# Kernel tuning notes

Hardware: AMD Instinct MI355X
Metric: run time of the kernel (lower is better)

The kernel has to match this reference:

```python
import jax, jax.numpy as jnp
import numpy as np

DIM = 64
B, H, W = 4, 80, 80


def setup_inputs() -> dict:
    key = jax.random.key(0)
    k1, k2, k3 = jax.random.split(key, 3)
    x = jax.random.normal(k1, (B, DIM, H, W), dtype=jnp.float32)
    # 1x1 conv == per-pixel linear: weight [3*dim, dim], bias [3*dim]
    w_qkv = jax.random.normal(k2, (3 * DIM, DIM), dtype=jnp.float32) * (1.0 / np.sqrt(DIM).astype(np.float32))
    b_qkv = jax.random.normal(k3, (3 * DIM,), dtype=jnp.float32) * 0.01
    return {"x": x, "w_qkv": w_qkv, "b_qkv": b_qkv}


def reference(x, w_qkv, b_qkv):
    Bb, C, Hh, Ww = x.shape
    N = Hh * Ww
    # 1x1 conv -> qkv, chunked along channels
    qkv = jnp.einsum('bchw,oc->bohw', x, w_qkv) + b_qkv[None, :, None, None]
    q, k, v = jnp.split(qkv, 3, axis=1)  # each [B,C,H,W]

    # --- spatial attention (uses q on both sides, as in the original) ---
    # qk: transpose(3,1) -> [B,W,H,C] -> [B, W*H, C]
    qk = jnp.transpose(q, (0, 3, 2, 1)).reshape(Bb, N, C)
    # kq: [B, C, H*W]  (note: different flatten order than qk, faithful to source)
    kq = q.reshape(Bb, C, N)
    ms = jax.nn.softmax(jnp.matmul(qk, kq), axis=-1)  # [B, N, N]

    # --- channel attention ---
    kf = k.reshape(Bb, C, N)                                # [B, C, N]
    qf = jnp.transpose(q, (0, 3, 2, 1)).reshape(Bb, N, C)   # [B, N, C]
    ma = jax.nn.softmax(jnp.matmul(kf, qf), axis=-1)        # [B, C, C]

    # --- apply to v ---
    vq = jnp.transpose(v, (0, 3, 2, 1)).reshape(Bb, N, C)   # [B, N, C]
    ms_out = jnp.matmul(ms, vq)                             # [B, N, C]
    ms_out = jnp.swapaxes(ms_out, 1, 2).reshape(Bb, C, Hh, Ww)
    ma_out = jnp.matmul(ma, v.reshape(Bb, C, N)).reshape(Bb, C, Hh, Ww)
    return ms_out + ma_out
```

## Files before the change

### kernel.cpp

```cpp
#include <hip/hip_runtime.h>
#include <stdint.h>

#define BATCH 4
#define CH 64
#define HW 80
#define NPIX 6400
#define SPLITS 3

typedef __attribute__((ext_vector_type(8))) short bf16x8;
typedef __attribute__((ext_vector_type(4))) float f32x4;

#define QSCALE 1.2011224087864498f
#define ESHIFT 115.41560327111707f

static __device__ __forceinline__ unsigned short f2bf(float f) {
  union { float f; unsigned int u; } v; v.f = f;
  unsigned int u = v.u;
  return (unsigned short)((u + 0x7fffu + ((u >> 16) & 1u)) >> 16);
}
static __device__ __forceinline__ float bf2f(unsigned short h) {
  union { unsigned int u; float f; } v; v.u = ((unsigned int)h) << 16;
  return v.f;
}
static __device__ __forceinline__ unsigned int split_pack(float a) {
  unsigned short hi = f2bf(a);
  union { unsigned int u; float f; } hf; hf.u = ((unsigned int)hi) << 16;
  unsigned short lo = f2bf(a - hf.f);
  return (unsigned int)hi | ((unsigned int)lo << 16);
}
static __device__ __forceinline__ void deint(uint4 a, uint4 b, bf16x8* h, bf16x8* l) {
  union { unsigned int u[4]; bf16x8 v; } H, L;
  H.u[0] = __builtin_amdgcn_perm(a.y, a.x, 0x05040100u);
  H.u[1] = __builtin_amdgcn_perm(a.w, a.z, 0x05040100u);
  H.u[2] = __builtin_amdgcn_perm(b.y, b.x, 0x05040100u);
  H.u[3] = __builtin_amdgcn_perm(b.w, b.z, 0x05040100u);
  L.u[0] = __builtin_amdgcn_perm(a.y, a.x, 0x07060302u);
  L.u[1] = __builtin_amdgcn_perm(a.w, a.z, 0x07060302u);
  L.u[2] = __builtin_amdgcn_perm(b.y, b.x, 0x07060302u);
  L.u[3] = __builtin_amdgcn_perm(b.w, b.z, 0x07060302u);
  *h = H.v; *l = L.v;
}

__global__ __launch_bounds__(512) void qkv_kernel(
    const float* __restrict__ x, const float* __restrict__ w,
    const float* __restrict__ bias, unsigned short* __restrict__ Qtbf,
    unsigned short* __restrict__ Vbf, unsigned int* __restrict__ Kpk,
    unsigned int* __restrict__ Qtn) {
  __shared__ float qs[64][65];
  int bid = blockIdx.x;
  int b = bid / 100, tile = bid % 100;
  int p0 = tile * 64;
  int t = threadIdx.x;
  int i = t & 63;
  int og = __builtin_amdgcn_readfirstlane(t >> 6);
  int p = p0 + i;
  int tp = (p % HW) * HW + p / HW;
  const float* xb = x + (size_t)b * CH * NPIX + p;
  float xv[64];
#pragma unroll
  for (int c = 0; c < 64; ++c) xv[c] = xb[(size_t)c * NPIX];
  size_t bc = (size_t)b * CH * NPIX;
  for (int j = 0; j < 24; j += 4) {
    int o = og * 24 + j;
    const float* wr0 = w + o * 64;
    const float* wr1 = wr0 + 64;
    const float* wr2 = wr0 + 128;
    const float* wr3 = wr0 + 192;
    float a0 = bias[o], a1 = bias[o + 1], a2 = bias[o + 2], a3 = bias[o + 3];
#pragma unroll
    for (int c = 0; c < 64; ++c) {
      float xc = xv[c];
      a0 += wr0[c] * xc;
      a1 += wr1[c] * xc;
      a2 += wr2[c] * xc;
      a3 += wr3[c] * xc;
    }
    float av[4] = {a0, a1, a2, a3};
#pragma unroll
    for (int u = 0; u < 4; ++u) {
      int oo = o + u;
      int cc = oo & 63;
      int kind = oo >> 6;
      float a = av[u];
      if (kind == 0) {
        qs[cc][i] = a;
        Qtn[bc + (size_t)cc * NPIX + tp] = split_pack(a);
      } else if (kind == 1) {
        Kpk[bc + (size_t)cc * NPIX + p] = split_pack(a);
      } else {
        Vbf[bc + (size_t)cc * NPIX + p] = f2bf(a);
      }
    }
  }
  __syncthreads();
  int j2 = t >> 3, g = t & 7;
  int pj = p0 + j2;
  int tpj = (pj % HW) * HW + pj / HW;
  unsigned int pk4[4];
#pragma unroll
  for (int q4 = 0; q4 < 4; ++q4) {
    float a0 = qs[g * 8 + q4 * 2][j2] * QSCALE;
    float a1 = qs[g * 8 + q4 * 2 + 1][j2] * QSCALE;
    pk4[q4] = (unsigned int)f2bf(a0) | ((unsigned int)f2bf(a1) << 16);
  }
  unsigned short* dst = Qtbf + ((size_t)b * NPIX + tpj) * 64 + g * 8;
  uint4 w0 = {pk4[0], pk4[1], pk4[2], pk4[3]};
  *(uint4*)&dst[0] = w0;
}

__global__ __launch_bounds__(256) void gram_kernel(
    const unsigned int* __restrict__ Kpk, const unsigned int* __restrict__ Qtn,
    float* __restrict__ Pc) {
  int bid = blockIdx.x;
  int b = bid / 100, chunk = bid % 100;
  int n0 = chunk * 64;
  int t = threadIdx.x;
  int w = t >> 6, lane = t & 63;
  int quad = lane >> 4, l16 = lane & 15;
  size_t bc = (size_t)b * CH * NPIX;

  f32x4 acc[4];
#pragma unroll
  for (int ct = 0; ct < 4; ++ct) acc[ct] = (f32x4){0.f, 0.f, 0.f, 0.f};

  const unsigned int* kp = Kpk + bc + (size_t)(w * 16 + l16) * NPIX + n0;
  bf16x8 ah[2], al[2];
#pragma unroll
  for (int ks2 = 0; ks2 < 2; ++ks2) {
    uint4 ua = *(const uint4*)&kp[ks2 * 32 + quad * 8];
    uint4 ub = *(const uint4*)&kp[ks2 * 32 + quad * 8 + 4];
    deint(ua, ub, &ah[ks2], &al[ks2]);
  }
#pragma unroll
  for (int ct = 0; ct < 4; ++ct) {
    const unsigned int* qp = Qtn + bc + (size_t)(ct * 16 + l16) * NPIX + n0;
#pragma unroll
    for (int ks2 = 0; ks2 < 2; ++ks2) {
      uint4 va = *(const uint4*)&qp[ks2 * 32 + quad * 8];
      uint4 vb = *(const uint4*)&qp[ks2 * 32 + quad * 8 + 4];
      bf16x8 bh, bl;
      deint(va, vb, &bh, &bl);
      acc[ct] = __builtin_amdgcn_mfma_f32_16x16x32_bf16(ah[ks2], bh, acc[ct], 0, 0, 0);
      acc[ct] = __builtin_amdgcn_mfma_f32_16x16x32_bf16(ah[ks2], bl, acc[ct], 0, 0, 0);
      acc[ct] = __builtin_amdgcn_mfma_f32_16x16x32_bf16(al[ks2], bh, acc[ct], 0, 0, 0);
    }
  }
#pragma unroll
  for (int ct = 0; ct < 4; ++ct)
#pragma unroll
    for (int r = 0; r < 4; ++r)
      atomicAdd(&Pc[((size_t)b * 64 + w * 16 + quad * 4 + r) * 64 + ct * 16 + l16],
                acc[ct][r]);
}

__global__ __launch_bounds__(256) void flash_kernel(
    const unsigned short* __restrict__ Qtbf, const unsigned short* __restrict__ Vbf,
    float* __restrict__ Opart, float* __restrict__ Lpart) {
  __shared__ char smem[40960] __attribute__((aligned(128)));

  int bid = blockIdx.x;
  int b = bid / 300;
  int rem = bid % 300;
  int qt = rem / 3, split = rem % 3;
  int p0 = qt * 64;
  int t = threadIdx.x;
  int w = t >> 6, lane = t & 63;
  int quad = lane >> 4, l16 = lane & 15;
  int sw = l16 & 7;
  size_t bq = (size_t)b * NPIX;
  size_t bC = (size_t)b * CH * NPIX;

  bf16x8 aq[2];
#pragma unroll
  for (int ks = 0; ks < 2; ++ks)
    aq[ks] = *(const bf16x8*)&Qtbf[(bq + p0 + w * 16 + l16) * 64 + ks * 32 + quad * 8];

  f32x4 oacc[4];
#pragma unroll
  for (int ct = 0; ct < 4; ++ct) oacc[ct] = (f32x4){0.f, 0.f, 0.f, 0.f};
  float psum = 0.f;

  const unsigned short* Kb = Qtbf + bq * 64;
  const unsigned short* Vb = Vbf + bC;
  int r0 = t >> 3, s0 = t & 7;
  int r1 = r0 + 32;
  int wOff0 = r0 * 64 + ((s0 ^ (r0 & 7)) << 3);
  int wOff1 = r1 * 64 + ((s0 ^ (r1 & 7)) << 3);

  int kt0 = split * 34;
  int niter = (split == 2) ? 32 : 34;

  unsigned short* Pw = (unsigned short*)(smem + 32768) + w * 16 * 64;

  uint4 kreg0, kreg1, vreg0, vreg1;
  {
    int n0 = kt0 * 64;
    kreg0 = *(const uint4*)&Kb[(size_t)(n0 + r0) * 64 + s0 * 8];
    vreg0 = *(const uint4*)&Vb[(size_t)r0 * NPIX + n0 + s0 * 8];
    kreg1 = *(const uint4*)&Kb[(size_t)(n0 + r1) * 64 + s0 * 8];
    vreg1 = *(const uint4*)&Vb[(size_t)r1 * NPIX + n0 + s0 * 8];
  }
  {
    unsigned short* K0 = (unsigned short*)smem;
    unsigned short* V0 = (unsigned short*)(smem + 16384);
    *(uint4*)&K0[wOff0] = kreg0;
    *(uint4*)&V0[wOff0] = vreg0;
    *(uint4*)&K0[wOff1] = kreg1;
    *(uint4*)&V0[wOff1] = vreg1;
  }
  {
    int n1 = (kt0 + 1) * 64;
    kreg0 = *(const uint4*)&Kb[(size_t)(n1 + r0) * 64 + s0 * 8];
    vreg0 = *(const uint4*)&Vb[(size_t)r0 * NPIX + n1 + s0 * 8];
    kreg1 = *(const uint4*)&Kb[(size_t)(n1 + r1) * 64 + s0 * 8];
    vreg1 = *(const uint4*)&Vb[(size_t)r1 * NPIX + n1 + s0 * 8];
  }
  __syncthreads();

  for (int it = 0; it < niter; ++it) {
    int cur = it & 1;
    unsigned short* Ksc = (unsigned short*)(smem + (cur << 13));
    unsigned short* Vsc = (unsigned short*)(smem + 16384 + (cur << 13));
    if (it + 1 < niter) {
      unsigned short* Kn = (unsigned short*)(smem + ((cur ^ 1) << 13));
      unsigned short* Vn = (unsigned short*)(smem + 16384 + ((cur ^ 1) << 13));
      *(uint4*)&Kn[wOff0] = kreg0;
      *(uint4*)&Vn[wOff0] = vreg0;
      *(uint4*)&Kn[wOff1] = kreg1;
      *(uint4*)&Vn[wOff1] = vreg1;
    }
    if (it + 2 < niter) {
      int n2 = (kt0 + it + 2) * 64;
      kreg0 = *(const uint4*)&Kb[(size_t)(n2 + r0) * 64 + s0 * 8];
      vreg0 = *(const uint4*)&Vb[(size_t)r0 * NPIX + n2 + s0 * 8];
      kreg1 = *(const uint4*)&Kb[(size_t)(n2 + r1) * 64 + s0 * 8];
      vreg1 = *(const uint4*)&Vb[(size_t)r1 * NPIX + n2 + s0 * 8];
    }
    f32x4 sc[4];
#pragma unroll
    for (int ct = 0; ct < 4; ++ct)
      sc[ct] = (f32x4){-ESHIFT, -ESHIFT, -ESHIFT, -ESHIFT};
    __builtin_amdgcn_s_setprio(1);
#pragma unroll
    for (int ks = 0; ks < 2; ++ks)
#pragma unroll
      for (int ct = 0; ct < 4; ++ct) {
        bf16x8 bk = *(const bf16x8*)&Ksc[(ct * 16 + l16) * 64 +
                                         (((ks * 4 + quad) ^ sw) << 3)];
        sc[ct] = __builtin_amdgcn_mfma_f32_16x16x32_bf16(bk, aq[ks], sc[ct], 0, 0, 0);
      }
    __builtin_amdgcn_s_setprio(0);
#pragma unroll
    for (int ct = 0; ct < 4; ++ct) {
      float e0 = __builtin_amdgcn_exp2f(sc[ct][0]);
      float e1 = __builtin_amdgcn_exp2f(sc[ct][1]);
      float e2 = __builtin_amdgcn_exp2f(sc[ct][2]);
      float e3 = __builtin_amdgcn_exp2f(sc[ct][3]);
      psum += (e0 + e1) + (e2 + e3);
      unsigned int pk0, pk1;
      asm("v_cvt_pk_bf16_f32 %0, %1, %2" : "=v"(pk0) : "v"(e0), "v"(e1));
      asm("v_cvt_pk_bf16_f32 %0, %1, %2" : "=v"(pk1) : "v"(e2), "v"(e3));
      uint2 pk = {pk0, pk1};
      *(uint2*)&Pw[l16 * 64 +
                   (((2 * ct + (quad >> 1)) ^ sw) << 3) + ((quad & 1) << 2)] = pk;
    }
    bf16x8 pf[2];
#pragma unroll
    for (int ks = 0; ks < 2; ++ks)
      pf[ks] = *(const bf16x8*)&Pw[l16 * 64 + (((ks * 4 + quad) ^ sw) << 3)];
    __builtin_amdgcn_s_setprio(1);
#pragma unroll
    for (int ks = 0; ks < 2; ++ks)
#pragma unroll
      for (int ct = 0; ct < 4; ++ct) {
        bf16x8 vf = *(const bf16x8*)&Vsc[(ct * 16 + l16) * 64 +
                                         (((ks * 4 + quad) ^ sw) << 3)];
        oacc[ct] = __builtin_amdgcn_mfma_f32_16x16x32_bf16(vf, pf[ks], oacc[ct], 0, 0, 0);
      }
    __builtin_amdgcn_s_setprio(0);
    __syncthreads();
  }
  float* Op = Opart + (size_t)(split * BATCH + b) * CH * NPIX;
  int pcol = p0 + w * 16 + l16;
  {
    float s = psum;
    s += __shfl_xor(s, 16, 64);
    s += __shfl_xor(s, 32, 64);
    if (quad == 0) Lpart[(size_t)(split * BATCH + b) * NPIX + pcol] = s;
  }
#pragma unroll
  for (int ct = 0; ct < 4; ++ct)
#pragma unroll
    for (int r = 0; r < 4; ++r)
      Op[(size_t)(ct * 16 + quad * 4 + r) * NPIX + pcol] = oacc[ct][r];
}

__global__ __launch_bounds__(256) void finalize_kernel(
    const float* __restrict__ Pc, const unsigned short* __restrict__ Vbf,
    const float* __restrict__ Opart, const float* __restrict__ Lpart,
    float* __restrict__ out) {
  __shared__ float maT[64 * 64];
  int bid = blockIdx.x;
  int b = bid / 100, nt = bid % 100;
  int t = threadIdx.x;
  if (t < 64) {
    int c = t;
    const float* row = Pc + ((size_t)b * 64 + c) * 64;
    float v[64];
    float mx = -1e30f;
#pragma unroll
    for (int j = 0; j < 64; ++j) { v[j] = row[j]; mx = fmaxf(mx, v[j]); }
    float s = 0.f;
#pragma unroll
    for (int j = 0; j < 64; ++j) { v[j] = __expf(v[j] - mx); s += v[j]; }
    float inv = 1.f / s;
#pragma unroll
    for (int j = 0; j < 64; ++j) maT[j * 64 + c] = v[j] * inv;
  }
  __syncthreads();
  int lane = t & 63, ct = t >> 6;
  int n = nt * 64 + lane;
  size_t bc = (size_t)b * CH * NPIX;
  const unsigned short* vb = Vbf + bc + n;
  float acc[16];
#pragma unroll
  for (int j = 0; j < 16; ++j) acc[j] = 0.f;
  for (int cp = 0; cp < 64; ++cp) {
    float vv = bf2f(vb[(size_t)cp * NPIX]);
    const float* m = &maT[cp * 64 + ct * 16];
    f32x4 m0 = *(const f32x4*)&m[0];
    f32x4 m1 = *(const f32x4*)&m[4];
    f32x4 m2 = *(const f32x4*)&m[8];
    f32x4 m3 = *(const f32x4*)&m[12];
#pragma unroll
    for (int j = 0; j < 4; ++j) {
      acc[j] += m0[j] * vv;
      acc[4 + j] += m1[j] * vv;
      acc[8 + j] += m2[j] * vv;
      acc[12 + j] += m3[j] * vv;
    }
  }
  float lsum = Lpart[(size_t)(0 * BATCH + b) * NPIX + n] +
               Lpart[(size_t)(1 * BATCH + b) * NPIX + n] +
               Lpart[(size_t)(2 * BATCH + b) * NPIX + n];
  float inv = 1.f / lsum;
  const float* O0 = Opart + (size_t)(0 * BATCH + b) * CH * NPIX;
  const float* O1 = Opart + (size_t)(1 * BATCH + b) * CH * NPIX;
  const float* O2 = Opart + (size_t)(2 * BATCH + b) * CH * NPIX;
#pragma unroll
  for (int j = 0; j < 16; ++j) {
    size_t co = (size_t)(ct * 16 + j) * NPIX + n;
    float o = O0[co] + O1[co] + O2[co];
    out[bc + co] = acc[j] + o * inv;
  }
}

extern "C" void kernel_launch(void* const* d_in, const int* in_sizes, int n_in,
                              void* d_out, int out_size, void* d_ws, size_t ws_size,
                              hipStream_t stream) {
  const float* x = (const float*)d_in[0];
  const float* w = (const float*)d_in[1];
  const float* bias = (const float*)d_in[2];
  float* out = (float*)d_out;
  char* ws = (char*)d_ws;
  unsigned short* Qtbf = (unsigned short*)(ws);
  unsigned short* Vbf = (unsigned short*)(ws + 3276800);
  unsigned int* Kpk = (unsigned int*)(ws + 6553600);
  unsigned int* Qtn = (unsigned int*)(ws + 13107200);
  float* Opart = (float*)(ws + 6553600);
  float* Pc = (float*)(ws + 26214400);
  float* Lpart = (float*)(ws + 26279936);

  hipMemsetAsync(Pc, 0, 65536, stream);
  qkv_kernel<<<400, 512, 0, stream>>>(x, w, bias, Qtbf, Vbf, Kpk, Qtn);
  gram_kernel<<<400, 256, 0, stream>>>(Kpk, Qtn, Pc);
  flash_kernel<<<1200, 256, 0, stream>>>(Qtbf, Vbf, Opart, Lpart);
  finalize_kernel<<<400, 256, 0, stream>>>(Pc, Vbf, Opart, Lpart, out);
}
```

Measured before the change: 177.9 us.

## Use direct global-to-LDS loads in flash kernel and split gram kernel finer

The flash kernel now fills its double-buffered K/V shared-memory tiles with global_load_lds instead of loading into registers and then writing to LDS. This removes the staging registers and the explicit LDS stores, and lets the prefetch overlap compute with less register pressure. The XOR swizzle moves into the global source addresses, so the destination layout matches the old one. Separately, the gram kernel processes 32 pixels per block across 800 blocks instead of 64 across 400, which adds parallelism at the cost of twice as many atomic adds.

```diff
diff --git a/kernel.cpp b/kernel.cpp
--- a/kernel.cpp
+++ b/kernel.cpp
@@ -39,6 +39,11 @@
   L.u[2] = __builtin_amdgcn_perm(b.y, b.x, 0x07060302u);
   L.u[3] = __builtin_amdgcn_perm(b.w, b.z, 0x07060302u);
   *h = H.v; *l = L.v;
+}
+static __device__ __forceinline__ void gload16(const unsigned short* g, char* l) {
+  __builtin_amdgcn_global_load_lds(
+      (const __attribute__((address_space(1))) unsigned int*)(g),
+      (__attribute__((address_space(3))) unsigned int*)(l), 16, 0, 0);
 }
 
 __global__ __launch_bounds__(512) void qkv_kernel(
@@ -112,8 +117,8 @@
     const unsigned int* __restrict__ Kpk, const unsigned int* __restrict__ Qtn,
     float* __restrict__ Pc) {
   int bid = blockIdx.x;
-  int b = bid / 100, chunk = bid % 100;
-  int n0 = chunk * 64;
+  int b = bid / 200, chunk = bid % 200;
+  int n0 = chunk * 32;
   int t = threadIdx.x;
   int w = t >> 6, lane = t & 63;
   int quad = lane >> 4, l16 = lane & 15;
@@ -124,26 +129,20 @@
   for (int ct = 0; ct < 4; ++ct) acc[ct] = (f32x4){0.f, 0.f, 0.f, 0.f};
 
   const unsigned int* kp = Kpk + bc + (size_t)(w * 16 + l16) * NPIX + n0;
-  bf16x8 ah[2], al[2];
-#pragma unroll
-  for (int ks2 = 0; ks2 < 2; ++ks2) {
-    uint4 ua = *(const uint4*)&kp[ks2 * 32 + quad * 8];
-    uint4 ub = *(const uint4*)&kp[ks2 * 32 + quad * 8 + 4];
-    deint(ua, ub, &ah[ks2], &al[ks2]);
-  }
+  uint4 ua = *(const uint4*)&kp[quad * 8];
+  uint4 ub = *(const uint4*)&kp[quad * 8 + 4];
+  bf16x8 ah, al;
+  deint(ua, ub, &ah, &al);
 #pragma unroll
   for (int ct = 0; ct < 4; ++ct) {
     const unsigned int* qp = Qtn + bc + (size_t)(ct * 16 + l16) * NPIX + n0;
-#pragma unroll
-    for (int ks2 = 0; ks2 < 2; ++ks2) {
-      uint4 va = *(const uint4*)&qp[ks2 * 32 + quad * 8];
-      uint4 vb = *(const uint4*)&qp[ks2 * 32 + quad * 8 + 4];
-      bf16x8 bh, bl;
-      deint(va, vb, &bh, &bl);
-      acc[ct] = __builtin_amdgcn_mfma_f32_16x16x32_bf16(ah[ks2], bh, acc[ct], 0, 0, 0);
-      acc[ct] = __builtin_amdgcn_mfma_f32_16x16x32_bf16(ah[ks2], bl, acc[ct], 0, 0, 0);
-      acc[ct] = __builtin_amdgcn_mfma_f32_16x16x32_bf16(al[ks2], bh, acc[ct], 0, 0, 0);
-    }
+    uint4 va = *(const uint4*)&qp[quad * 8];
+    uint4 vb = *(const uint4*)&qp[quad * 8 + 4];
+    bf16x8 bh, bl;
+    deint(va, vb, &bh, &bl);
+    acc[ct] = __builtin_amdgcn_mfma_f32_16x16x32_bf16(ah, bh, acc[ct], 0, 0, 0);
+    acc[ct] = __builtin_amdgcn_mfma_f32_16x16x32_bf16(ah, bl, acc[ct], 0, 0, 0);
+    acc[ct] = __builtin_amdgcn_mfma_f32_16x16x32_bf16(al, bh, acc[ct], 0, 0, 0);
   }
 #pragma unroll
   for (int ct = 0; ct < 4; ++ct)
@@ -182,60 +181,42 @@
 
   const unsigned short* Kb = Qtbf + bq * 64;
   const unsigned short* Vb = Vbf + bC;
-  int r0 = t >> 3, s0 = t & 7;
-  int r1 = r0 + 32;
-  int wOff0 = r0 * 64 + ((s0 ^ (r0 & 7)) << 3);
-  int wOff1 = r1 * 64 + ((s0 ^ (r1 & 7)) << 3);
+
+  int lr = lane >> 3, ls = lane & 7;
+  int colsw = (ls ^ lr) * 8;
+  int rA = w * 8 + lr;
+  int rB = 32 + w * 8 + lr;
+  int ldsA = __builtin_amdgcn_readfirstlane(w * 1024);
+  int ldsB = ldsA + 4096;
 
   int kt0 = split * 34;
   int niter = (split == 2) ? 32 : 34;
 
+  const unsigned short* gKA = Kb + (size_t)(kt0 * 64 + rA) * 64 + colsw;
+  const unsigned short* gKB = Kb + (size_t)(kt0 * 64 + rB) * 64 + colsw;
+  const unsigned short* gVA = Vb + (size_t)rA * NPIX + kt0 * 64 + colsw;
+  const unsigned short* gVB = Vb + (size_t)rB * NPIX + kt0 * 64 + colsw;
+
+  gload16(gKA, smem + ldsA);
+  gload16(gKB, smem + ldsB);
+  gload16(gVA, smem + 16384 + ldsA);
+  gload16(gVB, smem + 16384 + ldsB);
+  gKA += 64 * 64; gKB += 64 * 64; gVA += 64; gVB += 64;
+  __syncthreads();
+
   unsigned short* Pw = (unsigned short*)(smem + 32768) + w * 16 * 64;
-
-  uint4 kreg0, kreg1, vreg0, vreg1;
-  {
-    int n0 = kt0 * 64;
-    kreg0 = *(const uint4*)&Kb[(size_t)(n0 + r0) * 64 + s0 * 8];
-    vreg0 = *(const uint4*)&Vb[(size_t)r0 * NPIX + n0 + s0 * 8];
-    kreg1 = *(const uint4*)&Kb[(size_t)(n0 + r1) * 64 + s0 * 8];
-    vreg1 = *(const uint4*)&Vb[(size_t)r1 * NPIX + n0 + s0 * 8];
-  }
-  {
-    unsigned short* K0 = (unsigned short*)smem;
-    unsigned short* V0 = (unsigned short*)(smem + 16384);
-    *(uint4*)&K0[wOff0] = kreg0;
-    *(uint4*)&V0[wOff0] = vreg0;
-    *(uint4*)&K0[wOff1] = kreg1;
-    *(uint4*)&V0[wOff1] = vreg1;
-  }
-  {
-    int n1 = (kt0 + 1) * 64;
-    kreg0 = *(const uint4*)&Kb[(size_t)(n1 + r0) * 64 + s0 * 8];
-    vreg0 = *(const uint4*)&Vb[(size_t)r0 * NPIX + n1 + s0 * 8];
-    kreg1 = *(const uint4*)&Kb[(size_t)(n1 + r1) * 64 + s0 * 8];
-    vreg1 = *(const uint4*)&Vb[(size_t)r1 * NPIX + n1 + s0 * 8];
-  }
-  __syncthreads();
-
   for (int it = 0; it < niter; ++it) {
     int cur = it & 1;
+    if (it + 1 < niter) {
+      int off = (cur ^ 1) << 13;
+      gload16(gKA, smem + off + ldsA);
+      gload16(gKB, smem + off + ldsB);
+      gload16(gVA, smem + 16384 + off + ldsA);
+      gload16(gVB, smem + 16384 + off + ldsB);
+      gKA += 64 * 64; gKB += 64 * 64; gVA += 64; gVB += 64;
+    }
     unsigned short* Ksc = (unsigned short*)(smem + (cur << 13));
     unsigned short* Vsc = (unsigned short*)(smem + 16384 + (cur << 13));
-    if (it + 1 < niter) {
-      unsigned short* Kn = (unsigned short*)(smem + ((cur ^ 1) << 13));
-      unsigned short* Vn = (unsigned short*)(smem + 16384 + ((cur ^ 1) << 13));
-      *(uint4*)&Kn[wOff0] = kreg0;
-      *(uint4*)&Vn[wOff0] = vreg0;
-      *(uint4*)&Kn[wOff1] = kreg1;
-      *(uint4*)&Vn[wOff1] = vreg1;
-    }
-    if (it + 2 < niter) {
-      int n2 = (kt0 + it + 2) * 64;
-      kreg0 = *(const uint4*)&Kb[(size_t)(n2 + r0) * 64 + s0 * 8];
-      vreg0 = *(const uint4*)&Vb[(size_t)r0 * NPIX + n2 + s0 * 8];
-      kreg1 = *(const uint4*)&Kb[(size_t)(n2 + r1) * 64 + s0 * 8];
-      vreg1 = *(const uint4*)&Vb[(size_t)r1 * NPIX + n2 + s0 * 8];
-    }
     f32x4 sc[4];
 #pragma unroll
     for (int ct = 0; ct < 4; ++ct)
@@ -373,7 +354,7 @@
 
   hipMemsetAsync(Pc, 0, 65536, stream);
   qkv_kernel<<<400, 512, 0, stream>>>(x, w, bias, Qtbf, Vbf, Kpk, Qtn);
-  gram_kernel<<<400, 256, 0, stream>>>(Kpk, Qtn, Pc);
+  gram_kernel<<<800, 256, 0, stream>>>(Kpk, Qtn, Pc);
   flash_kernel<<<1200, 256, 0, stream>>>(Qtbf, Vbf, Opart, Lpart);
   finalize_kernel<<<400, 256, 0, stream>>>(Pc, Vbf, Opart, Lpart, out);
 }
```

Result: slower. 186.0 us (+4.6%).

## Use 2 waves with 32 query rows each and direct global-to-LDS loads in flash kernel

Applied to the files above, without the earlier changes.

The flash kernel now runs with 128 threads (2 waves) instead of 256. Each wave handles 32 query rows, so each K and V fragment read from LDS feeds two MFMAs. K/V tiles are copied straight into LDS with global_load_lds, which drops the register staging and the separate LDS store step. This should cut LDS read traffic per MFMA and VGPR pressure from prefetch registers. In exchange each block has fewer waves to hide latency, and the LDS writes now rely on buffer-load-to-LDS ordering under the existing barrier.

```diff
diff --git a/kernel.cpp b/kernel.cpp
--- a/kernel.cpp
+++ b/kernel.cpp
@@ -39,6 +39,11 @@
   L.u[2] = __builtin_amdgcn_perm(b.y, b.x, 0x07060302u);
   L.u[3] = __builtin_amdgcn_perm(b.w, b.z, 0x07060302u);
   *h = H.v; *l = L.v;
+}
+static __device__ __forceinline__ void gload16(const unsigned short* g, char* l) {
+  __builtin_amdgcn_global_load_lds(
+      (const __attribute__((address_space(1))) unsigned int*)(g),
+      (__attribute__((address_space(3))) unsigned int*)(l), 16, 0, 0);
 }
 
 __global__ __launch_bounds__(512) void qkv_kernel(
@@ -153,7 +158,7 @@
                 acc[ct][r]);
 }
 
-__global__ __launch_bounds__(256) void flash_kernel(
+__global__ __launch_bounds__(128) void flash_kernel(
     const unsigned short* __restrict__ Qtbf, const unsigned short* __restrict__ Vbf,
     float* __restrict__ Opart, float* __restrict__ Lpart) {
   __shared__ char smem[40960] __attribute__((aligned(128)));
@@ -170,76 +175,63 @@
   size_t bq = (size_t)b * NPIX;
   size_t bC = (size_t)b * CH * NPIX;
 
-  bf16x8 aq[2];
-#pragma unroll
-  for (int ks = 0; ks < 2; ++ks)
-    aq[ks] = *(const bf16x8*)&Qtbf[(bq + p0 + w * 16 + l16) * 64 + ks * 32 + quad * 8];
-
-  f32x4 oacc[4];
-#pragma unroll
-  for (int ct = 0; ct < 4; ++ct) oacc[ct] = (f32x4){0.f, 0.f, 0.f, 0.f};
-  float psum = 0.f;
+  bf16x8 aq[2][2];
+#pragma unroll
+  for (int mr = 0; mr < 2; ++mr)
+#pragma unroll
+    for (int ks = 0; ks < 2; ++ks)
+      aq[mr][ks] = *(const bf16x8*)&Qtbf[(bq + p0 + w * 32 + mr * 16 + l16) * 64 +
+                                         ks * 32 + quad * 8];
+
+  f32x4 oacc[2][4];
+#pragma unroll
+  for (int mr = 0; mr < 2; ++mr)
+#pragma unroll
+    for (int ct = 0; ct < 4; ++ct) oacc[mr][ct] = (f32x4){0.f, 0.f, 0.f, 0.f};
+  float psum[2] = {0.f, 0.f};
 
   const unsigned short* Kb = Qtbf + bq * 64;
   const unsigned short* Vb = Vbf + bC;
-  int r0 = t >> 3, s0 = t & 7;
-  int r1 = r0 + 32;
-  int wOff0 = r0 * 64 + ((s0 ^ (r0 & 7)) << 3);
-  int wOff1 = r1 * 64 + ((s0 ^ (r1 & 7)) << 3);
+
+  int lr = lane >> 3, ls = lane & 7;
+  int colsw = (ls ^ lr) * 8;
+  int rbase = w * 32 + lr;
+  int ldsW = __builtin_amdgcn_readfirstlane(w * 4096);
 
   int kt0 = split * 34;
   int niter = (split == 2) ? 32 : 34;
 
-  unsigned short* Pw = (unsigned short*)(smem + 32768) + w * 16 * 64;
-
-  uint4 kreg0, kreg1, vreg0, vreg1;
-  {
-    int n0 = kt0 * 64;
-    kreg0 = *(const uint4*)&Kb[(size_t)(n0 + r0) * 64 + s0 * 8];
-    vreg0 = *(const uint4*)&Vb[(size_t)r0 * NPIX + n0 + s0 * 8];
-    kreg1 = *(const uint4*)&Kb[(size_t)(n0 + r1) * 64 + s0 * 8];
-    vreg1 = *(const uint4*)&Vb[(size_t)r1 * NPIX + n0 + s0 * 8];
-  }
-  {
-    unsigned short* K0 = (unsigned short*)smem;
-    unsigned short* V0 = (unsigned short*)(smem + 16384);
-    *(uint4*)&K0[wOff0] = kreg0;
-    *(uint4*)&V0[wOff0] = vreg0;
-    *(uint4*)&K0[wOff1] = kreg1;
-    *(uint4*)&V0[wOff1] = vreg1;
-  }
-  {
-    int n1 = (kt0 + 1) * 64;
-    kreg0 = *(const uint4*)&Kb[(size_t)(n1 + r0) * 64 + s0 * 8];
-    vreg0 = *(const uint4*)&Vb[(size_t)r0 * NPIX + n1 + s0 * 8];
-    kreg1 = *(const uint4*)&Kb[(size_t)(n1 + r1) * 64 + s0 * 8];
-    vreg1 = *(const uint4*)&Vb[(size_t)r1 * NPIX + n1 + s0 * 8];
-  }
+  const unsigned short* gK = Kb + (size_t)(kt0 * 64 + rbase) * 64 + colsw;
+  const unsigned short* gV = Vb + (size_t)rbase * NPIX + kt0 * 64 + colsw;
+
+#pragma unroll
+  for (int c = 0; c < 4; ++c) {
+    gload16(gK + c * 512, smem + ldsW + c * 1024);
+    gload16(gV + (size_t)(c * 8) * NPIX, smem + 16384 + ldsW + c * 1024);
+  }
+  gK += 4096; gV += 64;
   __syncthreads();
 
+  unsigned short* Pw = (unsigned short*)(smem + 32768) + w * 2048;
   for (int it = 0; it < niter; ++it) {
     int cur = it & 1;
+    if (it + 1 < niter) {
+      int off = (cur ^ 1) << 13;
+#pragma unroll
+      for (int c = 0; c < 4; ++c) {
+        gload16(gK + c * 512, smem + off + ldsW + c * 1024);
+        gload16(gV + (size_t)(c * 8) * NPIX, smem + 16384 + off + ldsW + c * 1024);
+      }
+      gK += 4096; gV += 64;
+    }
     unsigned short* Ksc = (unsigned short*)(smem + (cur << 13));
     unsigned short* Vsc = (unsigned short*)(smem + 16384 + (cur << 13));
-    if (it + 1 < niter) {
-      unsigned short* Kn = (unsigned short*)(smem + ((cur ^ 1) << 13));
-      unsigned short* Vn = (unsigned short*)(smem + 16384 + ((cur ^ 1) << 13));
-      *(uint4*)&Kn[wOff0] = kreg0;
-      *(uint4*)&Vn[wOff0] = vreg0;
-      *(uint4*)&Kn[wOff1] = kreg1;
-      *(uint4*)&Vn[wOff1] = vreg1;
-    }
-    if (it + 2 < niter) {
-      int n2 = (kt0 + it + 2) * 64;
-      kreg0 = *(const uint4*)&Kb[(size_t)(n2 + r0) * 64 + s0 * 8];
-      vreg0 = *(const uint4*)&Vb[(size_t)r0 * NPIX + n2 + s0 * 8];
-      kreg1 = *(const uint4*)&Kb[(size_t)(n2 + r1) * 64 + s0 * 8];
-      vreg1 = *(const uint4*)&Vb[(size_t)r1 * NPIX + n2 + s0 * 8];
-    }
-    f32x4 sc[4];
-#pragma unroll
-    for (int ct = 0; ct < 4; ++ct)
-      sc[ct] = (f32x4){-ESHIFT, -ESHIFT, -ESHIFT, -ESHIFT};
+    f32x4 sc[2][4];
+#pragma unroll
+    for (int mr = 0; mr < 2; ++mr)
+#pragma unroll
+      for (int ct = 0; ct < 4; ++ct)
+        sc[mr][ct] = (f32x4){-ESHIFT, -ESHIFT, -ESHIFT, -ESHIFT};
     __builtin_amdgcn_s_setprio(1);
 #pragma unroll
     for (int ks = 0; ks < 2; ++ks)
@@ -247,27 +239,33 @@
       for (int ct = 0; ct < 4; ++ct) {
         bf16x8 bk = *(const bf16x8*)&Ksc[(ct * 16 + l16) * 64 +
                                          (((ks * 4 + quad) ^ sw) << 3)];
-        sc[ct] = __builtin_amdgcn_mfma_f32_16x16x32_bf16(bk, aq[ks], sc[ct], 0, 0, 0);
+        sc[0][ct] = __builtin_amdgcn_mfma_f32_16x16x32_bf16(bk, aq[0][ks], sc[0][ct], 0, 0, 0);
+        sc[1][ct] = __builtin_amdgcn_mfma_f32_16x16x32_bf16(bk, aq[1][ks], sc[1][ct], 0, 0, 0);
       }
     __builtin_amdgcn_s_setprio(0);
 #pragma unroll
-    for (int ct = 0; ct < 4; ++ct) {
-      float e0 = __builtin_amdgcn_exp2f(sc[ct][0]);
-      float e1 = __builtin_amdgcn_exp2f(sc[ct][1]);
-      float e2 = __builtin_amdgcn_exp2f(sc[ct][2]);
-      float e3 = __builtin_amdgcn_exp2f(sc[ct][3]);
-      psum += (e0 + e1) + (e2 + e3);
-      unsigned int pk0, pk1;
-      asm("v_cvt_pk_bf16_f32 %0, %1, %2" : "=v"(pk0) : "v"(e0), "v"(e1));
-      asm("v_cvt_pk_bf16_f32 %0, %1, %2" : "=v"(pk1) : "v"(e2), "v"(e3));
-      uint2 pk = {pk0, pk1};
-      *(uint2*)&Pw[l16 * 64 +
-                   (((2 * ct + (quad >> 1)) ^ sw) << 3) + ((quad & 1) << 2)] = pk;
-    }
-    bf16x8 pf[2];
-#pragma unroll
-    for (int ks = 0; ks < 2; ++ks)
-      pf[ks] = *(const bf16x8*)&Pw[l16 * 64 + (((ks * 4 + quad) ^ sw) << 3)];
+    for (int mr = 0; mr < 2; ++mr)
+#pragma unroll
+      for (int ct = 0; ct < 4; ++ct) {
+        float e0 = __builtin_amdgcn_exp2f(sc[mr][ct][0]);
+        float e1 = __builtin_amdgcn_exp2f(sc[mr][ct][1]);
+        float e2 = __builtin_amdgcn_exp2f(sc[mr][ct][2]);
+        float e3 = __builtin_amdgcn_exp2f(sc[mr][ct][3]);
+        psum[mr] += (e0 + e1) + (e2 + e3);
+        unsigned int pk0, pk1;
+        asm("v_cvt_pk_bf16_f32 %0, %1, %2" : "=v"(pk0) : "v"(e0), "v"(e1));
+        asm("v_cvt_pk_bf16_f32 %0, %1, %2" : "=v"(pk1) : "v"(e2), "v"(e3));
+        uint2 pk = {pk0, pk1};
+        *(uint2*)&Pw[(mr * 16 + l16) * 64 +
+                     (((2 * ct + (quad >> 1)) ^ sw) << 3) + ((quad & 1) << 2)] = pk;
+      }
+    bf16x8 pf[2][2];
+#pragma unroll
+    for (int mr = 0; mr < 2; ++mr)
+#pragma unroll
+      for (int ks = 0; ks < 2; ++ks)
+        pf[mr][ks] = *(const bf16x8*)&Pw[(mr * 16 + l16) * 64 +
+                                         (((ks * 4 + quad) ^ sw) << 3)];
     __builtin_amdgcn_s_setprio(1);
 #pragma unroll
     for (int ks = 0; ks < 2; ++ks)
@@ -275,24 +273,28 @@
       for (int ct = 0; ct < 4; ++ct) {
         bf16x8 vf = *(const bf16x8*)&Vsc[(ct * 16 + l16) * 64 +
                                          (((ks * 4 + quad) ^ sw) << 3)];
-        oacc[ct] = __builtin_amdgcn_mfma_f32_16x16x32_bf16(vf, pf[ks], oacc[ct], 0, 0, 0);
+        oacc[0][ct] = __builtin_amdgcn_mfma_f32_16x16x32_bf16(vf, pf[0][ks], oacc[0][ct], 0, 0, 0);
+        oacc[1][ct] = __builtin_amdgcn_mfma_f32_16x16x32_bf16(vf, pf[1][ks], oacc[1][ct], 0, 0, 0);
       }
     __builtin_amdgcn_s_setprio(0);
     __syncthreads();
   }
   float* Op = Opart + (size_t)(split * BATCH + b) * CH * NPIX;
-  int pcol = p0 + w * 16 + l16;
-  {
-    float s = psum;
+  int pcol = p0 + w * 32 + l16;
+#pragma unroll
+  for (int mr = 0; mr < 2; ++mr) {
+    float s = psum[mr];
     s += __shfl_xor(s, 16, 64);
     s += __shfl_xor(s, 32, 64);
-    if (quad == 0) Lpart[(size_t)(split * BATCH + b) * NPIX + pcol] = s;
-  }
-#pragma unroll
-  for (int ct = 0; ct < 4; ++ct)
-#pragma unroll
-    for (int r = 0; r < 4; ++r)
-      Op[(size_t)(ct * 16 + quad * 4 + r) * NPIX + pcol] = oacc[ct][r];
+    if (quad == 0) Lpart[(size_t)(split * BATCH + b) * NPIX + pcol + mr * 16] = s;
+  }
+#pragma unroll
+  for (int mr = 0; mr < 2; ++mr)
+#pragma unroll
+    for (int ct = 0; ct < 4; ++ct)
+#pragma unroll
+      for (int r = 0; r < 4; ++r)
+        Op[(size_t)(ct * 16 + quad * 4 + r) * NPIX + pcol + mr * 16] = oacc[mr][ct][r];
 }
 
 __global__ __launch_bounds__(256) void finalize_kernel(
@@ -374,6 +376,6 @@
   hipMemsetAsync(Pc, 0, 65536, stream);
   qkv_kernel<<<400, 512, 0, stream>>>(x, w, bias, Qtbf, Vbf, Kpk, Qtn);
   gram_kernel<<<400, 256, 0, stream>>>(Kpk, Qtn, Pc);
-  flash_kernel<<<1200, 256, 0, stream>>>(Qtbf, Vbf, Opart, Lpart);
+  flash_kernel<<<1200, 128, 0, stream>>>(Qtbf, Vbf, Opart, Lpart);
   finalize_kernel<<<400, 256, 0, stream>>>(Pc, Vbf, Opart, Lpart, out);
 }
```

After: 196.4 us. 1.1x slower.

## Compute QKV projection with split-bf16 MFMA instead of scalar FMA

Applied to the files above, without the earlier changes.

Rewrites the 1x1-conv QKV kernel to stage x tiles in swizzled shared memory as hi/lo bf16 pairs and compute the projection with 16x16x32 bf16 MFMAs, using three products (hh, hl, lh) to keep near-fp32 accuracy. The block drops from 512 to 256 threads, and each wave now owns three 16-channel output groups. The aim is to remove the scalar FMA cost and the strided per-thread x loads of the old version. The cost is extra shared memory, split/pack conversion work, and a small precision loss from the three-term emulation. This kernel is only one of four launches, so the effect on total time is limited.

```diff
diff --git a/kernel.cpp b/kernel.cpp
--- a/kernel.cpp
+++ b/kernel.cpp
@@ -41,71 +41,116 @@
   *h = H.v; *l = L.v;
 }
 
-__global__ __launch_bounds__(512) void qkv_kernel(
+__global__ __launch_bounds__(256) void qkv_kernel(
     const float* __restrict__ x, const float* __restrict__ w,
     const float* __restrict__ bias, unsigned short* __restrict__ Qtbf,
     unsigned short* __restrict__ Vbf, unsigned int* __restrict__ Kpk,
     unsigned int* __restrict__ Qtn) {
+  __shared__ unsigned short xh[64 * 64], xl[64 * 64];
   __shared__ float qs[64][65];
   int bid = blockIdx.x;
   int b = bid / 100, tile = bid % 100;
   int p0 = tile * 64;
   int t = threadIdx.x;
-  int i = t & 63;
-  int og = __builtin_amdgcn_readfirstlane(t >> 6);
-  int p = p0 + i;
-  int tp = (p % HW) * HW + p / HW;
-  const float* xb = x + (size_t)b * CH * NPIX + p;
-  float xv[64];
-#pragma unroll
-  for (int c = 0; c < 64; ++c) xv[c] = xb[(size_t)c * NPIX];
+  int w4 = __builtin_amdgcn_readfirstlane(t >> 6);
+  int lane = t & 63, quad = lane >> 4, l16 = lane & 15;
+  int sw = l16 & 7;
   size_t bc = (size_t)b * CH * NPIX;
-  for (int j = 0; j < 24; j += 4) {
-    int o = og * 24 + j;
-    const float* wr0 = w + o * 64;
-    const float* wr1 = wr0 + 64;
-    const float* wr2 = wr0 + 128;
-    const float* wr3 = wr0 + 192;
-    float a0 = bias[o], a1 = bias[o + 1], a2 = bias[o + 2], a3 = bias[o + 3];
-#pragma unroll
-    for (int c = 0; c < 64; ++c) {
-      float xc = xv[c];
-      a0 += wr0[c] * xc;
-      a1 += wr1[c] * xc;
-      a2 += wr2[c] * xc;
-      a3 += wr3[c] * xc;
-    }
-    float av[4] = {a0, a1, a2, a3};
-#pragma unroll
-    for (int u = 0; u < 4; ++u) {
-      int oo = o + u;
-      int cc = oo & 63;
-      int kind = oo >> 6;
-      float a = av[u];
-      if (kind == 0) {
-        qs[cc][i] = a;
-        Qtn[bc + (size_t)cc * NPIX + tp] = split_pack(a);
-      } else if (kind == 1) {
-        Kpk[bc + (size_t)cc * NPIX + p] = split_pack(a);
-      } else {
-        Vbf[bc + (size_t)cc * NPIX + p] = f2bf(a);
+
+  {
+    int cr = t >> 4;
+    int pb = (t & 15) * 4;
+#pragma unroll
+    for (int pass = 0; pass < 4; ++pass) {
+      int c = pass * 16 + cr;
+      float4 xv = *(const float4*)&x[bc + (size_t)c * NPIX + p0 + pb];
+      float vv[4] = {xv.x, xv.y, xv.z, xv.w};
+#pragma unroll
+      for (int e = 0; e < 4; ++e) {
+        int p = pb + e;
+        int addr = p * 64 + ((((c >> 3) ^ (p & 7))) << 3) + (c & 7);
+        unsigned int sp = split_pack(vv[e]);
+        xh[addr] = (unsigned short)sp;
+        xl[addr] = (unsigned short)(sp >> 16);
       }
     }
   }
+  bf16x8 wh[3][2], wl[3][2];
+  f32x4 acc[3][4];
+#pragma unroll
+  for (int oi = 0; oi < 3; ++oi) {
+    int och = w4 * 3 + oi;
+#pragma unroll
+    for (int ks = 0; ks < 2; ++ks) {
+      const float* wr = w + (size_t)(och * 16 + l16) * 64 + ks * 32 + quad * 8;
+      float4 f0 = *(const float4*)&wr[0];
+      float4 f1 = *(const float4*)&wr[4];
+      uint4 a4, b4;
+      a4.x = split_pack(f0.x); a4.y = split_pack(f0.y);
+      a4.z = split_pack(f0.z); a4.w = split_pack(f0.w);
+      b4.x = split_pack(f1.x); b4.y = split_pack(f1.y);
+      b4.z = split_pack(f1.z); b4.w = split_pack(f1.w);
+      deint(a4, b4, &wh[oi][ks], &wl[oi][ks]);
+    }
+    f32x4 bv = *(const f32x4*)&bias[och * 16 + quad * 4];
+#pragma unroll
+    for (int pch = 0; pch < 4; ++pch) acc[oi][pch] = bv;
+  }
   __syncthreads();
-  int j2 = t >> 3, g = t & 7;
-  int pj = p0 + j2;
+#pragma unroll
+  for (int ks = 0; ks < 2; ++ks)
+#pragma unroll
+    for (int pch = 0; pch < 4; ++pch) {
+      int xoff = (pch * 16 + l16) * 64 + (((ks * 4 + quad) ^ sw) << 3);
+      bf16x8 bh = *(const bf16x8*)&xh[xoff];
+      bf16x8 bl = *(const bf16x8*)&xl[xoff];
+#pragma unroll
+      for (int oi = 0; oi < 3; ++oi) {
+        acc[oi][pch] = __builtin_amdgcn_mfma_f32_16x16x32_bf16(wh[oi][ks], bh, acc[oi][pch], 0, 0, 0);
+        acc[oi][pch] = __builtin_amdgcn_mfma_f32_16x16x32_bf16(wh[oi][ks], bl, acc[oi][pch], 0, 0, 0);
+        acc[oi][pch] = __builtin_amdgcn_mfma_f32_16x16x32_bf16(wl[oi][ks], bh, acc[oi][pch], 0, 0, 0);
+      }
+    }
+#pragma unroll
+  for (int oi = 0; oi < 3; ++oi) {
+    int och = w4 * 3 + oi;
+    int kind = och >> 2;
+#pragma unroll
+    for (int pch = 0; pch < 4; ++pch) {
+      int p = p0 + pch * 16 + l16;
+      int tp = (p % HW) * HW + p / HW;
+#pragma unroll
+      for (int r = 0; r < 4; ++r) {
+        int o = och * 16 + quad * 4 + r;
+        int cc = o & 63;
+        float a = acc[oi][pch][r];
+        if (kind == 0) {
+          qs[cc][pch * 16 + l16] = a;
+          Qtn[bc + (size_t)cc * NPIX + tp] = split_pack(a);
+        } else if (kind == 1) {
+          Kpk[bc + (size_t)cc * NPIX + p] = split_pack(a);
+        } else {
+          Vbf[bc + (size_t)cc * NPIX + p] = f2bf(a);
+        }
+      }
+    }
+  }
+  __syncthreads();
+  int j = t >> 2, g = t & 3;
+  int pj = p0 + j;
   int tpj = (pj % HW) * HW + pj / HW;
-  unsigned int pk4[4];
-#pragma unroll
-  for (int q4 = 0; q4 < 4; ++q4) {
-    float a0 = qs[g * 8 + q4 * 2][j2] * QSCALE;
-    float a1 = qs[g * 8 + q4 * 2 + 1][j2] * QSCALE;
-    pk4[q4] = (unsigned int)f2bf(a0) | ((unsigned int)f2bf(a1) << 16);
-  }
-  unsigned short* dst = Qtbf + ((size_t)b * NPIX + tpj) * 64 + g * 8;
-  uint4 w0 = {pk4[0], pk4[1], pk4[2], pk4[3]};
+  unsigned int pk8[8];
+#pragma unroll
+  for (int q4 = 0; q4 < 8; ++q4) {
+    float a0 = qs[g * 16 + q4 * 2][j] * QSCALE;
+    float a1 = qs[g * 16 + q4 * 2 + 1][j] * QSCALE;
+    pk8[q4] = (unsigned int)f2bf(a0) | ((unsigned int)f2bf(a1) << 16);
+  }
+  unsigned short* dst = Qtbf + ((size_t)b * NPIX + tpj) * 64 + g * 16;
+  uint4 w0 = {pk8[0], pk8[1], pk8[2], pk8[3]};
+  uint4 w1 = {pk8[4], pk8[5], pk8[6], pk8[7]};
   *(uint4*)&dst[0] = w0;
+  *(uint4*)&dst[8] = w1;
 }
 
 __global__ __launch_bounds__(256) void gram_kernel(
@@ -372,7 +417,7 @@
   float* Lpart = (float*)(ws + 26279936);
 
   hipMemsetAsync(Pc, 0, 65536, stream);
-  qkv_kernel<<<400, 512, 0, stream>>>(x, w, bias, Qtbf, Vbf, Kpk, Qtn);
+  qkv_kernel<<<400, 256, 0, stream>>>(x, w, bias, Qtbf, Vbf, Kpk, Qtn);
   gram_kernel<<<400, 256, 0, stream>>>(Kpk, Qtn, Pc);
   flash_kernel<<<1200, 256, 0, stream>>>(Qtbf, Vbf, Opart, Lpart);
   finalize_kernel<<<400, 256, 0, stream>>>(Pc, Vbf, Opart, Lpart, out);
```

Result: no change. 179.5 us (+0.9%).
